# Optimization experiments

Measured on AMD Instinct MI355X. Metric: run time of the kernel, lower is better.

## Reference

```python
import jax, jax.numpy as jnp
import numpy as np

B, S = 64, 512
VOCAB, D_FEATS, D_HID = 1000, 64, 256


def setup_inputs() -> dict:
    key = jax.random.key(0)
    ks = jax.random.split(key, 12)
    s = 0.05  # keep tanh RNN in a sane dynamic range
    return {
        "batch": jax.random.randint(ks[0], (B, S), 0, VOCAB),
        "features": jax.random.normal(ks[1], (VOCAB, D_FEATS), jnp.float32),
        "W_ih0": jax.random.normal(ks[2], (D_HID, D_FEATS), jnp.float32) * s,
        "W_hh0": jax.random.normal(ks[3], (D_HID, D_HID), jnp.float32) * s,
        "b_ih0": jax.random.normal(ks[4], (D_HID,), jnp.float32) * s,
        "b_hh0": jax.random.normal(ks[5], (D_HID,), jnp.float32) * s,
        "W_ih1": jax.random.normal(ks[6], (D_HID, D_HID), jnp.float32) * s,
        "W_hh1": jax.random.normal(ks[7], (D_HID, D_HID), jnp.float32) * s,
        "b_ih1": jax.random.normal(ks[8], (D_HID,), jnp.float32) * s,
        "b_hh1": jax.random.normal(ks[9], (D_HID,), jnp.float32) * s,
        "W_out": jax.random.normal(ks[10], (VOCAB, D_HID), jnp.float32) * s,
        "b_out": jax.random.normal(ks[11], (VOCAB,), jnp.float32) * s,
    }


def _rnn_layer(x, W_ih, W_hh, b_ih, b_hh):
    # x: [B, S, F] -> [B, S, H]; tanh RNN as in torch.nn.RNN:
    # h_t = tanh(x_t @ W_ih^T + b_ih + h_{t-1} @ W_hh^T + b_hh)
    xp = jnp.einsum("bsf,hf->bsh", x, W_ih) + b_ih + b_hh  # precompute input part
    h0 = jnp.zeros((x.shape[0], W_hh.shape[0]), x.dtype)

    def step(h, xt):  # xt: [B, H]
        h = jnp.tanh(xt + h @ W_hh.T)
        return h, h

    _, hs = jax.lax.scan(step, h0, jnp.swapaxes(xp, 0, 1))  # [S, B, H]
    return jnp.swapaxes(hs, 0, 1)


def reference(batch, features, W_ih0, W_hh0, b_ih0, b_hh0,
              W_ih1, W_hh1, b_ih1, b_hh1, W_out, b_out):
    # Vectorized replacement for the Python double-loop gather:
    x = features[batch]  # [B, S, num_feats]
    h = _rnn_layer(x, W_ih0, W_hh0, b_ih0, b_hh0)
    h = _rnn_layer(h, W_ih1, W_hh1, b_ih1, b_hh1)
    return jnp.einsum("bsh,vh->bsv", h, W_out) + b_out  # logits [B, S, vocab]
```

## Files before the change

kernel.cpp:

```cpp
#include <hip/hip_runtime.h>
#include <hip/hip_bf16.h>

#define NB 64
#define NS 512
#define NV 1000
#define NF 64
#define NH 256

typedef short bf16x8 __attribute__((ext_vector_type(8)));
typedef float f32x4 __attribute__((ext_vector_type(4)));

__device__ __forceinline__ float bf2f(unsigned int u16bits){
    union { unsigned int i; float f; } v;
    v.i = (u16bits & 0xffffu) << 16;
    return v.f;
}

__device__ __forceinline__ float tanh_fast(float x){
    float e = __builtin_amdgcn_exp2f(x * 2.8853900817779268f);
    return 1.f - 2.f * __builtin_amdgcn_rcpf(e + 1.f);
}

__device__ __forceinline__ bool detect_f32(const void* probe){
    const unsigned short* p = (const unsigned short*)probe;
    bool bad = false; float mx = 0.f;
#pragma unroll
    for (int j = 0; j < 64; ++j){
        float v = fabsf(bf2f(p[j]));
        bad = bad || !(v == v);
        mx = fmaxf(mx, v);
    }
    return bad || (mx > 100.f);
}

struct ConvArgs { const void* src[11]; __hip_bfloat16* dst[11]; int n[11]; };

__global__ void k_conv_all(ConvArgs a, const void* __restrict__ probe){
    const int seg = blockIdx.y;
    const int n = a.n[seg];
    int i = blockIdx.x * 256 + threadIdx.x;
    if (i >= n) return;
    const bool f32in = detect_f32(probe);
    const int stride = gridDim.x * 256;
    __hip_bfloat16* dst = a.dst[seg];
    if (f32in){
        const float* s = (const float*)a.src[seg];
        for (; i < n; i += stride) dst[i] = __float2bfloat16(s[i]);
    } else {
        const unsigned short* s = (const unsigned short*)a.src[seg];
        for (; i < n; i += stride) dst[i] = __float2bfloat16(bf2f(s[i]));
    }
}

__global__ void k_pre0(const __hip_bfloat16* __restrict__ feats,
                       const __hip_bfloat16* __restrict__ Wih,
                       const __hip_bfloat16* __restrict__ bih,
                       const __hip_bfloat16* __restrict__ bhh,
                       __hip_bfloat16* __restrict__ pre0){
    const int v = blockIdx.x, h = threadIdx.x;
    __shared__ __align__(16) float fsh[NF];
    if (h < NF) fsh[h] = __bfloat162float(feats[v*NF + h]);
    __syncthreads();
    const uint4* wr = reinterpret_cast<const uint4*>(Wih + h*NF);
    float acc = __bfloat162float(bih[h]) + __bfloat162float(bhh[h]);
#pragma unroll
    for (int j = 0; j < 8; ++j){
        uint4 q = wr[j];
        const float* hf = &fsh[j*8];
        acc += hf[0]*bf2f(q.x) + hf[1]*bf2f(q.x>>16)
             + hf[2]*bf2f(q.y) + hf[3]*bf2f(q.y>>16)
             + hf[4]*bf2f(q.z) + hf[5]*bf2f(q.z>>16)
             + hf[6]*bf2f(q.w) + hf[7]*bf2f(q.w>>16);
    }
    pre0[v*NH + h] = __float2bfloat16(acc);
}

#define BAR() do { asm volatile("s_waitcnt lgkmcnt(0)" ::: "memory");  \
                   __builtin_amdgcn_s_barrier();                        \
                   asm volatile("" ::: "memory"); } while (0)

#define PHASE(WF, BOFF, ACC)                                                      \
  _Pragma("unroll") for (int kc = 0; kc < 2; ++kc){                               \
    bf16x8 hfa[4];                                                                \
    _Pragma("unroll") for (int j = 0; j < 4; ++j)                                 \
      hfa[j] = *reinterpret_cast<const bf16x8*>(                                  \
          ldsb + (BOFF) + roffb + (kc*4 + j)*1024);                               \
    _Pragma("unroll") for (int j = 0; j < 4; ++j){                                \
      ACC[0] = __builtin_amdgcn_mfma_f32_16x16x32_bf16(WF[0][kc*4+j], hfa[j], ACC[0],0,0,0); \
      ACC[1] = __builtin_amdgcn_mfma_f32_16x16x32_bf16(WF[1][kc*4+j], hfa[j], ACC[1],0,0,0); \
    }                                                                             \
  }

#define PHASER(WF, HARR, ACC)                                                     \
  _Pragma("unroll") for (int ks = 0; ks < 8; ++ks){                               \
    ACC[0] = __builtin_amdgcn_mfma_f32_16x16x32_bf16(WF[0][ks], HARR[ks], ACC[0],0,0,0); \
    ACC[1] = __builtin_amdgcn_mfma_f32_16x16x32_bf16(WF[1][ks], HARR[ks], ACC[1],0,0,0); \
  }

#define TANH_PACK_STORE(ACC, WOFF, GSTORE, SPAR)                                  \
  _Pragma("unroll") for (int nt = 0; nt < 2; ++nt){                               \
    float t0 = tanh_fast(ACC[nt][0]), t1 = tanh_fast(ACC[nt][1]);                 \
    float t2 = tanh_fast(ACC[nt][2]), t3 = tanh_fast(ACC[nt][3]);                 \
    unsigned plo, phi;                                                            \
    asm("v_cvt_pk_bf16_f32 %0, %1, %2" : "=v"(plo) : "v"(t0), "v"(t1));           \
    asm("v_cvt_pk_bf16_f32 %0, %1, %2" : "=v"(phi) : "v"(t2), "v"(t3));           \
    uint2 p; p.x = plo; p.y = phi;                                                \
    *reinterpret_cast<uint2*>(ldsb + (WOFF) + woffb + nt*512) = p;                \
    if (GSTORE) *reinterpret_cast<uint2*>(hop + (SPAR)*NH + nt*16) = p;           \
  }

#define STEP(R0, W0, R1, W1, XS, IREG, SPAR)                                      \
  do {                                                                            \
    bf16x8 hC[8];                                                                 \
    _Pragma("unroll") for (int ks = 0; ks < 8; ++ks)                              \
      hC[ks] = *reinterpret_cast<const bf16x8*>(ldsb + (R1) + roffb + ks*1024);   \
    f32x4 acc0[2];                                                                \
    _Pragma("unroll") for (int nt = 0; nt < 2; ++nt)                              \
      _Pragma("unroll") for (int r = 0; r < 4; ++r)                               \
        acc0[nt][r] = bf2f(((const unsigned short*)&XS[nt])[r]);                  \
    { const unsigned short* gb = pre0b + (size_t)IREG*NH + cq;                    \
      XS[0] = *reinterpret_cast<const ushort4*>(gb);                              \
      XS[1] = *reinterpret_cast<const ushort4*>(gb + 16);                         \
      int sn = s + (SPAR) + 4; sn = (sn < NS) ? sn : NS - 1;                      \
      IREG = batch_g[sn]; }                                                       \
    PHASE(wf0, R0, acc0);                                                         \
    TANH_PACK_STORE(acc0, W0, 0, SPAR);                                           \
    BAR();                                                                        \
    f32x4 acc1[2]; acc1[0] = biasv[0]; acc1[1] = biasv[1];                        \
    PHASER(wf1, hC, acc1);                                                        \
    PHASE(wfG, W0, acc1);                                                         \
    TANH_PACK_STORE(acc1, W1, 1, SPAR);                                           \
    BAR();                                                                        \
  } while (0)

__global__ __launch_bounds__(512, 2) void k_rnn_fused(
        const int* __restrict__ batch,
        const unsigned short* __restrict__ pre0b,
        const __hip_bfloat16* __restrict__ Whh0,
        const __hip_bfloat16* __restrict__ Wih1,
        const __hip_bfloat16* __restrict__ Whh1,
        const __hip_bfloat16* __restrict__ bih1,
        const __hip_bfloat16* __restrict__ bhh1,
        __hip_bfloat16* __restrict__ hout){
    const int l  = threadIdx.x & 63;
    const int w  = threadIdx.x >> 6;
    const int b0 = blockIdx.x * 16;
    const int lr = l & 15;
    const int kq = l >> 4;
    const int c0 = w * 32;
    const int cq = c0 + kq*4;

    bf16x8 wf0[2][8], wfG[2][8], wf1[2][8];
#pragma unroll
    for (int nt = 0; nt < 2; ++nt)
#pragma unroll
        for (int ks = 0; ks < 8; ++ks){
            const size_t o = (size_t)(c0 + nt*16 + lr)*NH + ks*32 + kq*8;
            wf0[nt][ks] = *reinterpret_cast<const bf16x8*>(Whh0 + o);
            wfG[nt][ks] = *reinterpret_cast<const bf16x8*>(Wih1 + o);
            wf1[nt][ks] = *reinterpret_cast<const bf16x8*>(Whh1 + o);
            asm volatile("" : "+v"(wf0[nt][ks]));
            asm volatile("" : "+v"(wfG[nt][ks]));
            asm volatile("" : "+v"(wf1[nt][ks]));
        }

    f32x4 biasv[2];
#pragma unroll
    for (int nt = 0; nt < 2; ++nt)
#pragma unroll
        for (int r = 0; r < 4; ++r){
            int c = cq + nt*16 + r;
            biasv[nt][r] = __bfloat162float(bih1[c]) + __bfloat162float(bhh1[c]);
        }

    __shared__ __align__(16) char lds_all[32768];
    char* ldsb = lds_all;
    *reinterpret_cast<uint4*>(ldsb + threadIdx.x*16)         = uint4{0,0,0,0};
    *reinterpret_cast<uint4*>(ldsb + 16384 + threadIdx.x*16) = uint4{0,0,0,0};

    const int roffb = kq*256 + lr*16;
    const int woffb = (cq >> 3)*256 + lr*16 + (cq & 7)*2;

    const int* batch_g = batch + (size_t)(b0 + lr)*NS;
    __hip_bfloat16* hop = hout + ((size_t)(b0+lr)*NS)*NH + cq;

    ushort4 xA[2], xB[2]; int iA, iB;
    {
        int j0 = batch_g[0], j1 = batch_g[1];
        const unsigned short* g0 = pre0b + (size_t)j0*NH + cq;
        const unsigned short* g1 = pre0b + (size_t)j1*NH + cq;
        xA[0] = *reinterpret_cast<const ushort4*>(g0);
        xA[1] = *reinterpret_cast<const ushort4*>(g0 + 16);
        xB[0] = *reinterpret_cast<const ushort4*>(g1);
        xB[1] = *reinterpret_cast<const ushort4*>(g1 + 16);
        iA = batch_g[2]; iB = batch_g[3];
    }
    __syncthreads();

    for (int s = 0; s < NS; s += 2){
        STEP(0,    8192, 16384, 24576, xA, iA, 0);
        STEP(8192, 0,    24576, 16384, xB, iB, 1);
        hop += 2*NH;
    }
}

template<int N>
__global__ __launch_bounds__(256, 2) void k_gemm_big(
        const __hip_bfloat16* __restrict__ A,
        const __hip_bfloat16* __restrict__ W,
        const __hip_bfloat16* __restrict__ bias,
        void* __restrict__ Cout, int ldc,
        const void* __restrict__ probe){
    const bool f32out = detect_f32(probe);
    const int m0 = blockIdx.x * 256;
    const int n0 = blockIdx.y * 64;
    const int wv = threadIdx.x >> 6;
    const int l  = threadIdx.x & 63;
    const int lr = l & 15;
    const int kb = (l >> 4) * 8;

    bf16x8 wfr[4][8];
#pragma unroll
    for (int nt = 0; nt < 4; ++nt){
        int ncol = n0 + nt*16 + lr;
        int nc = (ncol < N) ? ncol : (N-1);
#pragma unroll
        for (int ks = 0; ks < 8; ++ks){
            wfr[nt][ks] = *reinterpret_cast<const bf16x8*>(
                W + (size_t)nc*NH + ks*32 + kb);
            asm volatile("" : "+v"(wfr[nt][ks]));
        }
    }

    float bsum[4];
#pragma unroll
    for (int nt = 0; nt < 4; ++nt){
        int ncol = n0 + nt*16 + lr;
        bsum[nt] = (ncol < N) ? __bfloat162float(bias[ncol]) : 0.f;
    }

#pragma unroll
    for (int mt = 0; mt < 4; ++mt){
        const int mrow = m0 + mt*64 + wv*16 + lr;
        bf16x8 af[8];
#pragma unroll
        for (int ks = 0; ks < 8; ++ks)
            af[ks] = *reinterpret_cast<const bf16x8*>(
                A + (size_t)mrow*NH + ks*32 + kb);
        f32x4 acc[4] = {};
#pragma unroll
        for (int ks = 0; ks < 8; ++ks){
#pragma unroll
            for (int nt = 0; nt < 4; ++nt)
                acc[nt] = __builtin_amdgcn_mfma_f32_16x16x32_bf16(
                    af[ks], wfr[nt][ks], acc[nt], 0, 0, 0);
        }
#pragma unroll
        for (int nt = 0; nt < 4; ++nt){
            int ncol = n0 + nt*16 + lr;
            if (ncol >= N) continue;
#pragma unroll
            for (int r = 0; r < 4; ++r){
                int row = m0 + mt*64 + wv*16 + (l>>4)*4 + r;
                float val = acc[nt][r] + bsum[nt];
                if (f32out) ((float*)Cout)[(size_t)row*ldc + ncol] = val;
                else        ((__hip_bfloat16*)Cout)[(size_t)row*ldc + ncol] = __float2bfloat16(val);
            }
        }
    }
}

extern "C" void kernel_launch(void* const* d_in, const int* in_sizes, int n_in,
                              void* d_out, int out_size, void* d_ws, size_t ws_size,
                              hipStream_t stream){
    const int* batch = (const int*)d_in[0];
    const void* probe = d_in[3];

    char* ws = (char*)d_ws;
    size_t off = 0;
    auto give = [&](size_t bytes)->char*{
        char* p = ws + off; off = (off + bytes + 511) & ~(size_t)511; return p;
    };
    __hip_bfloat16* cFeats = (__hip_bfloat16*)give(2*NV*NF);
    __hip_bfloat16* cWih0  = (__hip_bfloat16*)give(2*NH*NF);
    __hip_bfloat16* cWhh0  = (__hip_bfloat16*)give(2*NH*NH);
    __hip_bfloat16* cBih0  = (__hip_bfloat16*)give(2*NH);
    __hip_bfloat16* cBhh0  = (__hip_bfloat16*)give(2*NH);
    __hip_bfloat16* cWih1  = (__hip_bfloat16*)give(2*NH*NH);
    __hip_bfloat16* cWhh1  = (__hip_bfloat16*)give(2*NH*NH);
    __hip_bfloat16* cBih1  = (__hip_bfloat16*)give(2*NH);
    __hip_bfloat16* cBhh1  = (__hip_bfloat16*)give(2*NH);
    __hip_bfloat16* cWout  = (__hip_bfloat16*)give(2*NV*NH);
    __hip_bfloat16* cBout  = (__hip_bfloat16*)give(2*NV);
    __hip_bfloat16* pre0b  = (__hip_bfloat16*)give(2*NV*NH + 64);
    __hip_bfloat16* hbuf   = (__hip_bfloat16*)give(2*(size_t)NB*NS*NH);

    ConvArgs ca;
    const void* srcs[11] = { d_in[1], d_in[2], d_in[3], d_in[4], d_in[5], d_in[6],
                             d_in[7], d_in[8], d_in[9], d_in[10], d_in[11] };
    __hip_bfloat16* dsts[11] = { cFeats, cWih0, cWhh0, cBih0, cBhh0, cWih1,
                                 cWhh1, cBih1, cBhh1, cWout, cBout };
    int ns[11] = { NV*NF, NH*NF, NH*NH, NH, NH, NH*NH, NH*NH, NH, NH, NV*NH, NV };
    for (int i = 0; i < 11; ++i){ ca.src[i] = srcs[i]; ca.dst[i] = dsts[i]; ca.n[i] = ns[i]; }
    k_conv_all<<<dim3(64, 11), dim3(256), 0, stream>>>(ca, probe);

    k_pre0<<<dim3(NV), dim3(256), 0, stream>>>(cFeats, cWih0, cBih0, cBhh0, pre0b);
    k_rnn_fused<<<dim3(NB/16), dim3(512), 0, stream>>>(
        batch, (const unsigned short*)pre0b, cWhh0, cWih1, cWhh1, cBih1, cBhh1, hbuf);
    k_gemm_big<NV><<<dim3((NB*NS)/256, 16), dim3(256), 0, stream>>>(
        hbuf, cWout, cBout, d_out, NV, probe);
}
```

Before: 747.7 us.

## Skew two RNN layers by one timestep to use a single barrier per step

Restructures the fused two-layer RNN loop so layer 0 at step t and layer 1 at step t-1 run in the same phase. Both read the previous layer-0 hidden state from LDS, so their MFMAs interleave, and each step needs one barrier instead of two. This removes a barrier and a serialized dependency from each timestep of the latency-bound recurrence. It adds a prologue/epilogue iteration (257 pairs) with a guard on the layer-1 store, and zeroes all four LDS buffers.

After: 756.2 us. Within noise of the previous version (+1.1%).

```diff
diff --git a/kernel.cpp b/kernel.cpp
--- a/kernel.cpp
+++ b/kernel.cpp
@@ -79,41 +79,13 @@
                    __builtin_amdgcn_s_barrier();                        \
                    asm volatile("" ::: "memory"); } while (0)
 
-#define PHASE(WF, BOFF, ACC)                                                      \
-  _Pragma("unroll") for (int kc = 0; kc < 2; ++kc){                               \
-    bf16x8 hfa[4];                                                                \
-    _Pragma("unroll") for (int j = 0; j < 4; ++j)                                 \
-      hfa[j] = *reinterpret_cast<const bf16x8*>(                                  \
-          ldsb + (BOFF) + roffb + (kc*4 + j)*1024);                               \
-    _Pragma("unroll") for (int j = 0; j < 4; ++j){                                \
-      ACC[0] = __builtin_amdgcn_mfma_f32_16x16x32_bf16(WF[0][kc*4+j], hfa[j], ACC[0],0,0,0); \
-      ACC[1] = __builtin_amdgcn_mfma_f32_16x16x32_bf16(WF[1][kc*4+j], hfa[j], ACC[1],0,0,0); \
-    }                                                                             \
-  }
-
-#define PHASER(WF, HARR, ACC)                                                     \
-  _Pragma("unroll") for (int ks = 0; ks < 8; ++ks){                               \
-    ACC[0] = __builtin_amdgcn_mfma_f32_16x16x32_bf16(WF[0][ks], HARR[ks], ACC[0],0,0,0); \
-    ACC[1] = __builtin_amdgcn_mfma_f32_16x16x32_bf16(WF[1][ks], HARR[ks], ACC[1],0,0,0); \
-  }
-
-#define TANH_PACK_STORE(ACC, WOFF, GSTORE, SPAR)                                  \
-  _Pragma("unroll") for (int nt = 0; nt < 2; ++nt){                               \
-    float t0 = tanh_fast(ACC[nt][0]), t1 = tanh_fast(ACC[nt][1]);                 \
-    float t2 = tanh_fast(ACC[nt][2]), t3 = tanh_fast(ACC[nt][3]);                 \
-    unsigned plo, phi;                                                            \
-    asm("v_cvt_pk_bf16_f32 %0, %1, %2" : "=v"(plo) : "v"(t0), "v"(t1));           \
-    asm("v_cvt_pk_bf16_f32 %0, %1, %2" : "=v"(phi) : "v"(t2), "v"(t3));           \
-    uint2 p; p.x = plo; p.y = phi;                                                \
-    *reinterpret_cast<uint2*>(ldsb + (WOFF) + woffb + nt*512) = p;                \
-    if (GSTORE) *reinterpret_cast<uint2*>(hop + (SPAR)*NH + nt*16) = p;           \
-  }
-
-#define STEP(R0, W0, R1, W1, XS, IREG, SPAR)                                      \
+#define MFMA16(A, B, C) __builtin_amdgcn_mfma_f32_16x16x32_bf16(A, B, C, 0, 0, 0)
+
+#define STEP(RH0, WH0, RH1, WH1, XS, IREG, S)                                     \
   do {                                                                            \
-    bf16x8 hC[8];                                                                 \
+    bf16x8 hC[8];                                                    \
     _Pragma("unroll") for (int ks = 0; ks < 8; ++ks)                              \
-      hC[ks] = *reinterpret_cast<const bf16x8*>(ldsb + (R1) + roffb + ks*1024);   \
+      hC[ks] = *reinterpret_cast<const bf16x8*>(ldsb + (RH1) + roffb + ks*1024);  \
     f32x4 acc0[2];                                                                \
     _Pragma("unroll") for (int nt = 0; nt < 2; ++nt)                              \
       _Pragma("unroll") for (int r = 0; r < 4; ++r)                               \
@@ -121,15 +93,46 @@
     { const unsigned short* gb = pre0b + (size_t)IREG*NH + cq;                    \
       XS[0] = *reinterpret_cast<const ushort4*>(gb);                              \
       XS[1] = *reinterpret_cast<const ushort4*>(gb + 16);                         \
-      int sn = s + (SPAR) + 4; sn = (sn < NS) ? sn : NS - 1;                      \
+      int sn = (S) + 5; sn = (sn < NS) ? sn : NS - 1;                             \
       IREG = batch_g[sn]; }                                                       \
-    PHASE(wf0, R0, acc0);                                                         \
-    TANH_PACK_STORE(acc0, W0, 0, SPAR);                                           \
-    BAR();                                                                        \
     f32x4 acc1[2]; acc1[0] = biasv[0]; acc1[1] = biasv[1];                        \
-    PHASER(wf1, hC, acc1);                                                        \
-    PHASE(wfG, W0, acc1);                                                         \
-    TANH_PACK_STORE(acc1, W1, 1, SPAR);                                           \
+    _Pragma("unroll") for (int kc = 0; kc < 2; ++kc){                             \
+      bf16x8 hfa[4];                       \
+      _Pragma("unroll") for (int j = 0; j < 4; ++j)                               \
+        hfa[j] = *reinterpret_cast<const bf16x8*>(                                \
+            ldsb + (RH0) + roffb + (kc*4 + j)*1024);                              \
+      _Pragma("unroll") for (int j = 0; j < 4; ++j){                              \
+        acc0[0] = MFMA16(wf0[0][kc*4+j], hfa[j], acc0[0]);                        \
+        acc0[1] = MFMA16(wf0[1][kc*4+j], hfa[j], acc0[1]);                        \
+        acc1[0] = MFMA16(wfG[0][kc*4+j], hfa[j], acc1[0]);                        \
+        acc1[1] = MFMA16(wfG[1][kc*4+j], hfa[j], acc1[1]);                        \
+      }                                                                           \
+    }                                                                             \
+    _Pragma("unroll") for (int ks = 0; ks < 8; ++ks){                             \
+      acc1[0] = MFMA16(wf1[0][ks], hC[ks], acc1[0]);                              \
+      acc1[1] = MFMA16(wf1[1][ks], hC[ks], acc1[1]);                              \
+    }                                                                             \
+    _Pragma("unroll") for (int nt = 0; nt < 2; ++nt){           \
+      float t0 = tanh_fast(acc0[nt][0]), t1 = tanh_fast(acc0[nt][1]);             \
+      float t2 = tanh_fast(acc0[nt][2]), t3 = tanh_fast(acc0[nt][3]);             \
+      unsigned plo, phi;                                                          \
+      asm("v_cvt_pk_bf16_f32 %0, %1, %2" : "=v"(plo) : "v"(t0), "v"(t1));         \
+      asm("v_cvt_pk_bf16_f32 %0, %1, %2" : "=v"(phi) : "v"(t2), "v"(t3));         \
+      uint2 p; p.x = plo; p.y = phi;                                              \
+      *reinterpret_cast<uint2*>(ldsb + (WH0) + woffb + nt*512) = p;               \
+    }                                                                             \
+    if ((unsigned)(S) < NS){                     \
+      _Pragma("unroll") for (int nt = 0; nt < 2; ++nt){                           \
+        float t0 = tanh_fast(acc1[nt][0]), t1 = tanh_fast(acc1[nt][1]);           \
+        float t2 = tanh_fast(acc1[nt][2]), t3 = tanh_fast(acc1[nt][3]);           \
+        unsigned plo, phi;                                                        \
+        asm("v_cvt_pk_bf16_f32 %0, %1, %2" : "=v"(plo) : "v"(t0), "v"(t1));       \
+        asm("v_cvt_pk_bf16_f32 %0, %1, %2" : "=v"(phi) : "v"(t2), "v"(t3));       \
+        uint2 p; p.x = plo; p.y = phi;                                            \
+        *reinterpret_cast<uint2*>(ldsb + (WH1) + woffb + nt*512) = p;             \
+        *reinterpret_cast<uint2*>(hob + ((size_t)(S) << 8) + nt*16) = p;          \
+      }                                                                           \
+    }                                                                             \
     BAR();                                                                        \
   } while (0)
 
@@ -175,14 +178,16 @@
 
     __shared__ __align__(16) char lds_all[32768];
     char* ldsb = lds_all;
-    *reinterpret_cast<uint4*>(ldsb + threadIdx.x*16)         = uint4{0,0,0,0};
-    *reinterpret_cast<uint4*>(ldsb + 16384 + threadIdx.x*16) = uint4{0,0,0,0};
+    *reinterpret_cast<uint4*>(ldsb + threadIdx.x*16)          = uint4{0,0,0,0};
+    *reinterpret_cast<uint4*>(ldsb + 8192  + threadIdx.x*16)  = uint4{0,0,0,0};
+    *reinterpret_cast<uint4*>(ldsb + 16384 + threadIdx.x*16)  = uint4{0,0,0,0};
+    *reinterpret_cast<uint4*>(ldsb + 24576 + threadIdx.x*16)  = uint4{0,0,0,0};
 
     const int roffb = kq*256 + lr*16;
     const int woffb = (cq >> 3)*256 + lr*16 + (cq & 7)*2;
 
     const int* batch_g = batch + (size_t)(b0 + lr)*NS;
-    __hip_bfloat16* hop = hout + ((size_t)(b0+lr)*NS)*NH + cq;
+    __hip_bfloat16* hob = hout + ((size_t)(b0+lr)*NS)*NH + cq;
 
     ushort4 xA[2], xB[2]; int iA, iB;
     {
@@ -197,10 +202,10 @@
     }
     __syncthreads();
 
-    for (int s = 0; s < NS; s += 2){
-        STEP(0,    8192, 16384, 24576, xA, iA, 0);
-        STEP(8192, 0,    24576, 16384, xB, iB, 1);
-        hop += 2*NH;
+    for (int p = 0; p < 257; ++p){
+        const int t = p*2;
+        STEP(8192, 0,     16384, 24576, xA, iA, t-1);
+        STEP(0,    8192,  24576, 16384, xB, iB, t);
     }
 }
 
```
